# Kernel optimization log

Hardware: AMD Instinct MI355X
Metric: run time of the kernel (lower is better)

Reference implementation:

```python
import jax, jax.numpy as jnp
import numpy as np
from jax import lax

P = 128   # patch_size
S = 64    # stride
K = 31    # PSF kernel size
NZ = 15   # number of Zernike coefficients
HID = 64  # aberration MLP hidden width


def setup_inputs() -> dict:
    key = jax.random.key(0)
    ks = jax.random.split(key, 8)
    B, C, H, W = 8, 3, 512, 512
    x_hat = jax.random.uniform(ks[0], (B, C, H, W), dtype=jnp.float32)
    w1 = jax.random.normal(ks[1], (2, HID), dtype=jnp.float32) * 0.5
    b1 = jnp.zeros((HID,), jnp.float32)
    w2 = jax.random.normal(ks[2], (HID, HID), dtype=jnp.float32) * 0.125
    b2 = jnp.zeros((HID,), jnp.float32)
    w3 = jax.random.normal(ks[3], (HID, NZ), dtype=jnp.float32) * 0.1
    b3 = jnp.zeros((NZ,), jnp.float32)
    zernike_basis = jax.random.normal(ks[4], (NZ, K, K), dtype=jnp.float32) * 0.5
    return {"x_hat": x_hat, "w1": w1, "b1": b1, "w2": w2, "b2": b2,
            "w3": w3, "b3": b3, "zernike_basis": zernike_basis}


def _hann(n):
    # torch.hann_window (periodic=True): 0.5*(1 - cos(2*pi*k/n))
    return 0.5 - 0.5 * jnp.cos(2.0 * jnp.pi * jnp.arange(n, dtype=jnp.float32) / n)


def _psf_from_coeffs(coeffs, basis):
    # coeffs: [N, NZ], basis: [NZ, K, K] -> normalized PSFs [N, K, K]
    phase = jnp.einsum('nz,zhw->nhw', coeffs, basis)          # [N, K, K]
    g = jnp.linspace(-1.0, 1.0, K, dtype=jnp.float32)
    r2 = g[:, None] ** 2 + g[None, :] ** 2
    mask = (r2 <= 1.0).astype(jnp.float32)                    # circular pupil
    pupil = mask * jnp.exp(1j * phase.astype(jnp.complex64))
    field = jnp.fft.fftshift(jnp.fft.fft2(jnp.fft.ifftshift(pupil, axes=(-2, -1))), axes=(-2, -1))
    psf = jnp.abs(field) ** 2
    psf = psf / (jnp.sum(psf, axis=(-2, -1), keepdims=True) + 1e-12)
    return psf


def _forward(x_hat, w1, b1, w2, b2, w3, b3, basis):
    B, C, H, W = x_hat.shape
    pad_h = (S - (H - P) % S) % S
    pad_w = (S - (W - P) % S) % S
    x = jnp.pad(x_hat, ((0, 0), (0, 0), (0, pad_h), (0, pad_w)), mode='reflect') \
        if (pad_h or pad_w) else x_hat
    H_pad, W_pad = x.shape[2], x.shape[3]
    n_h = (H_pad - P) // S + 1
    n_w = (W_pad - P) // S + 1
    N = n_h * n_w

    # ---- unfold into overlapping patches: [B*N, C, P, P] ----
    r0 = jnp.arange(n_h) * S
    c0 = jnp.arange(n_w) * S
    ridx = r0[:, None] + jnp.arange(P)[None, :]               # [n_h, P]
    cidx = c0[:, None] + jnp.arange(P)[None, :]               # [n_w, P]
    patches = x[:, :, ridx[:, None, :, None], cidx[None, :, None, :]]  # [B,C,n_h,n_w,P,P]
    patches = patches.transpose(0, 2, 3, 1, 4, 5).reshape(B * N, C, P, P)

    # ---- per-patch normalized center coords in [-1, 1] ----
    y_norm = (r0.astype(jnp.float32) + P / 2.0) / H_pad * 2.0 - 1.0
    x_norm = (c0.astype(jnp.float32) + P / 2.0) / W_pad * 2.0 - 1.0
    gy, gx = jnp.meshgrid(y_norm, x_norm, indexing='ij')
    coords = jnp.stack([gy, gx], axis=-1).reshape(N, 2)       # [N, 2]
    coords = jnp.tile(coords, (B, 1))                         # [B*N, 2]

    # ---- aberration MLP -> Zernike coeffs -> PSF kernels ----
    h = jax.nn.relu(coords @ w1 + b1)
    h = jax.nn.relu(h @ w2 + b2)
    coeffs = h @ w3 + b3                                      # [B*N, NZ]
    psf = _psf_from_coeffs(coeffs, basis)                     # [B*N, K, K], C_k = 1
    kf = psf[:, ::-1, ::-1]                                   # flip -> true convolution

    # ---- spatially varying per-patch conv (C>1, C_k==1 broadcast branch) ----
    BN = B * N
    pad = K // 2
    xp = jnp.pad(patches, ((0, 0), (0, 0), (pad, pad), (pad, pad)))
    lhs = xp.reshape(1, BN * C, P + 2 * pad, P + 2 * pad)
    rhs = jnp.broadcast_to(kf[:, None, :, :], (BN, C, K, K)).reshape(BN * C, 1, K, K)
    y = lax.conv_general_dilated(lhs, rhs, (1, 1), 'VALID',
                                 dimension_numbers=('NCHW', 'OIHW', 'NCHW'),
                                 feature_group_count=BN * C)
    y_patches = y.reshape(BN, C, P, P)

    # ---- Hann window + overlap-add fold ----
    hann = _hann(P)
    window = hann[:, None] * hann[None, :]                    # [P, P]
    y_patches = y_patches * window[None, None]

    idx = (ridx[:, None, :, None] * W_pad + cidx[None, :, None, :]).reshape(-1)  # [N*P*P]
    vals = y_patches.reshape(B, N, C, P, P).transpose(0, 2, 1, 3, 4).reshape(B, C, -1)
    y_accum = jnp.zeros((B, C, H_pad * W_pad), jnp.float32).at[:, :, idx].add(vals)
    y_accum = y_accum.reshape(B, C, H_pad, W_pad)

    wvals = jnp.broadcast_to(window, (N, P, P)).reshape(-1)
    w_accum = jnp.zeros((H_pad * W_pad,), jnp.float32).at[idx].add(wvals)
    w_accum = w_accum.reshape(1, 1, H_pad, W_pad)

    y_hat = y_accum / (w_accum + 1e-8)
    return y_hat[:, :, :H, :W]


def reference(x_hat, w1, b1, w2, b2, w3, b3, zernike_basis):
    return _forward(x_hat, w1, b1, w2, b2, w3, b3, zernike_basis)
```

## Files before the change

kernel.cpp:

```cpp
#include <hip/hip_runtime.h>
#include <math.h>

#define B_ 8
#define C_ 3
#define HW_ 512
#define P_ 128
#define S_ 64
#define K_ 31
#define NZ_ 15
#define HID_ 64
#define NPOS_ 49
#define BN_ (B_*NPOS_)

#define LROWB_ 384
#define TROWS_ 160
#define FRAG_U32_ 256
#define NSTEP_ 16
#define BPOS_U32_ (NSTEP_ * 3 * FRAG_U32_)

typedef __attribute__((ext_vector_type(8))) short bf16x8;
typedef __attribute__((ext_vector_type(4))) float f32x4;

__device__ __forceinline__ float hann128(int p) {
    return 0.5f - 0.5f * cosf(6.283185307179586f * (float)p / 128.0f);
}

__device__ __forceinline__ unsigned int bf16_rne(float f) {
    union { float f; unsigned int u; } v; v.f = f;
    unsigned int r = v.u + 0x7fffu + ((v.u >> 16) & 1u);
    return r >> 16;
}

__device__ __forceinline__ float bf16_to_f(unsigned int bits16) {
    union { unsigned int u; float f; } v; v.u = bits16 << 16;
    return v.f;
}

__global__ __launch_bounds__(1024) void psf_kernel(
    const float* __restrict__ w1, const float* __restrict__ b1,
    const float* __restrict__ w2, const float* __restrict__ b2,
    const float* __restrict__ w3, const float* __restrict__ b3,
    const float* __restrict__ basis, unsigned int* __restrict__ bfrags)
{
    __shared__ float h1[HID_], h2[HID_], coef[NZ_];
    __shared__ float pupR[961], pupI[961], tR[961], tI[961];
    __shared__ float rootR[31], rootI[31];
    __shared__ float red[16];
    int n = blockIdx.x;
    int nh = n / 7, nw = n % 7;
    int tid = threadIdx.x;
    float cy = (float)(nh * S_ + P_ / 2) * (2.0f / (float)HW_) - 1.0f;
    float cx = (float)(nw * S_ + P_ / 2) * (2.0f / (float)HW_) - 1.0f;

    if (tid < HID_) h1[tid] = fmaxf(0.0f, cy * w1[tid] + cx * w1[HID_ + tid] + b1[tid]);
    if (tid < 31) {
        float ang = -6.283185307179586f * (float)tid / 31.0f;
        rootR[tid] = cosf(ang);
        rootI[tid] = sinf(ang);
    }
    __syncthreads();
    if (tid < HID_) {
        float s = b2[tid];
        for (int k = 0; k < HID_; ++k) s = fmaf(h1[k], w2[k * HID_ + tid], s);
        h2[tid] = fmaxf(0.0f, s);
    }
    __syncthreads();
    if (tid < NZ_) {
        float s = b3[tid];
        for (int k = 0; k < HID_; ++k) s = fmaf(h2[k], w3[k * NZ_ + tid], s);
        coef[tid] = s;
    }
    __syncthreads();

    for (int idx = tid; idx < 961; idx += 1024) {
        int h = idx / 31, w = idx % 31;
        float ph = 0.0f;
        for (int z = 0; z < NZ_; ++z) ph = fmaf(coef[z], basis[z * 961 + idx], ph);
        int dh = h - 15, dw = w - 15;
        bool m = (dh * dh + dw * dw) <= 225;
        float sv, cv;
        sincosf(ph, &sv, &cv);
        pupR[idx] = m ? cv : 0.0f;
        pupI[idx] = m ? sv : 0.0f;
    }
    __syncthreads();

    for (int idx = tid; idx < 961; idx += 1024) {
        int h = idx / 31, k = idx % 31;
        float ar = 0.0f, ai = 0.0f;
        for (int w = 0; w < 31; ++w) {
            int tt = (k * w) % 31;
            float cr = rootR[tt], ci = rootI[tt];
            float pr = pupR[h * 31 + w], pi = pupI[h * 31 + w];
            ar += pr * cr - pi * ci;
            ai += pr * ci + pi * cr;
        }
        tR[idx] = ar; tI[idx] = ai;
    }
    __syncthreads();

    float lsum = 0.0f;
    for (int idx = tid; idx < 961; idx += 1024) {
        int u = idx / 31, k = idx % 31;
        float gr = 0.0f, gi = 0.0f;
        for (int h = 0; h < 31; ++h) {
            int tt = (u * h) % 31;
            float cr = rootR[tt], ci = rootI[tt];
            float ar = tR[h * 31 + k], ai = tI[h * 31 + k];
            gr += ar * cr - ai * ci;
            gi += ar * ci + ai * cr;
        }
        float p = gr * gr + gi * gi;
        pupR[idx] = p;
        lsum += p;
    }
    float v = lsum;
    #pragma unroll
    for (int off = 32; off >= 1; off >>= 1) v += __shfl_xor(v, off, 64);
    if ((tid & 63) == 0) red[tid >> 6] = v;
    __syncthreads();
    if (tid == 0) {
        float s = 0.0f;
        #pragma unroll
        for (int i = 0; i < 16; ++i) s += red[i];
        red[0] = 1.0f / (s + 1e-12f);
    }
    __syncthreads();
    float inv = red[0];
    for (int idx = tid; idx < 961; idx += 1024) {
        int j = idx / 31, i = idx % 31;
        int u = (15 - j + 31) % 31, vv = (15 - i + 31) % 31;
        tI[idx] = pupR[u * 31 + vv] * inv;
    }
    __syncthreads();

    unsigned int* bf = bfrags + (size_t)n * BPOS_U32_;
    for (int w2 = tid; w2 < BPOS_U32_; w2 += 1024) {
        int jc = w2 >> 8;
        int s = jc / 3, c = jc % 3;
        int rem = w2 & 255;
        int l = rem >> 2, ew = rem & 3;
        int nn = l & 15, kg = l >> 4;
        unsigned int pack = 0;
        #pragma unroll
        for (int q = 0; q < 2; ++q) {
            int e = ew * 2 + q;
            int kk = kg * 8 + e;
            int jrow = 2 * s + (kk >> 4);
            int tap = 16 * c + (kk & 15) - nn;
            float vx = (jrow >= 1 && jrow <= 31 && tap >= 1 && tap <= 31)
                       ? tI[(jrow - 1) * 31 + (tap - 1)] : 0.0f;
            pack |= bf16_rne(vx) << (16 * q);
        }
        bf[w2] = pack;
    }
}

template<int MODE>
__global__ __launch_bounds__(512, 4) void conv_mfma_kernel(
    const float* __restrict__ x, const unsigned int* __restrict__ bfrags,
    void* __restrict__ dst)
{
    __shared__ unsigned short sIn[TROWS_ * (LROWB_ / 2)];
    __shared__ float sH[128];

    int t = blockIdx.x;
    int cc = t % 3;
    int bn = t / 3;
    int b = bn / NPOS_, n = bn % NPOS_;
    int nh = n / 7, nw = n % 7;
    int r0 = nh * S_, c0 = nw * S_;
    int tid = threadIdx.x;

    if (tid < 128) sH[tid] = hann128(tid);

    const float* xb = x + ((size_t)(b * C_ + cc) * HW_ + r0) * HW_ + c0;
    for (int i = tid; i < TROWS_ * 24; i += 512) {
        int r = i / 24, jj = i % 24;
        uint4 o = make_uint4(0u, 0u, 0u, 0u);
        if (r >= 16 && r < 144 && jj >= 2 && jj <= 17) {
            const float* rp = &xb[(r - 16) * HW_ + (jj * 8 - 16)];
            float4 v0 = *(const float4*)rp;
            float4 v1 = *(const float4*)(rp + 4);
            o.x = bf16_rne(v0.x) | (bf16_rne(v0.y) << 16);
            o.y = bf16_rne(v0.z) | (bf16_rne(v0.w) << 16);
            o.z = bf16_rne(v1.x) | (bf16_rne(v1.y) << 16);
            o.w = bf16_rne(v1.z) | (bf16_rne(v1.w) << 16);
        }
        int byteoff = (r * LROWB_ + jj * 16) ^ ((r & 7) << 4);
        *(uint4*)((char*)sIn + byteoff) = o;
    }
    __syncthreads();

    int lane = tid & 63, wv = tid >> 6;
    int m0 = wv * 16;
    int lrow = lane & 15, lkg = lane >> 4;

    f32x4 acc[8];
    #pragma unroll
    for (int q = 0; q < 8; ++q) acc[q] = (f32x4){0.f, 0.f, 0.f, 0.f};

    int rowb = m0 + lrow + (lkg >> 1);
    int colb = (lkg & 1) * 16;
    const bf16x8* bpos = (const bf16x8*)(bfrags + (size_t)n * BPOS_U32_) + lane;
    int sbase = wv * 2;

    int ss0 = sbase & 15;
    bf16x8 Bc0 = bpos[ss0 * 192], Bc1 = bpos[ss0 * 192 + 64], Bc2 = bpos[ss0 * 192 + 128];

    #pragma unroll 2
    for (int s = 0; s < NSTEP_; ++s) {
        int ss = (s + sbase) & 15;
        bf16x8 Bn0, Bn1, Bn2;
        if (s + 1 < NSTEP_) {
            int ssn = (s + 1 + sbase) & 15;
            const bf16x8* bp = bpos + ssn * 192;
            Bn0 = bp[0]; Bn1 = bp[64]; Bn2 = bp[128];
        } else { Bn0 = Bc0; Bn1 = Bc1; Bn2 = Bc2; }

        int r2 = rowb + 2 * ss;
        int base = r2 * LROWB_ + colb;
        int xorv = (r2 & 7) << 4;
        bf16x8 A[10];
        #pragma unroll
        for (int p = 0; p < 10; ++p)
            A[p] = *(const bf16x8*)((const char*)sIn + ((base + p * 32) ^ xorv));

        __builtin_amdgcn_s_setprio(1);
        #pragma unroll
        for (int q = 0; q < 8; ++q) {
            acc[q] = __builtin_amdgcn_mfma_f32_16x16x32_bf16(A[q],     Bc0, acc[q], 0, 0, 0);
            acc[q] = __builtin_amdgcn_mfma_f32_16x16x32_bf16(A[q + 1], Bc1, acc[q], 0, 0, 0);
            acc[q] = __builtin_amdgcn_mfma_f32_16x16x32_bf16(A[q + 2], Bc2, acc[q], 0, 0, 0);
        }
        __builtin_amdgcn_s_setprio(0);
        Bc0 = Bn0; Bc1 = Bn1; Bc2 = Bn2;
    }

    int prow0 = m0 + lkg * 4;
    float hy[4];
    #pragma unroll
    for (int r = 0; r < 4; ++r) hy[r] = sH[prow0 + r];

    #pragma unroll
    for (int q = 0; q < 8; ++q) {
        int pcol = 16 * q + lrow;
        float hxv = sH[pcol];
        #pragma unroll
        for (int r = 0; r < 4; ++r) {
            int prow = prow0 + r;
            float val = acc[q][r] * hy[r] * hxv;
            if (MODE == 0) {
                unsigned short* yp = (unsigned short*)dst + (((size_t)bn * C_ + cc) << 14);
                yp[prow * P_ + pcol] = (unsigned short)bf16_rne(val);
            } else {
                float* ob = (float*)dst;
                atomicAdd(ob + ((size_t)(b * C_ + cc) * HW_ + r0 + prow) * HW_ + c0 + pcol, val);
            }
        }
    }
}

__global__ __launch_bounds__(256) void gather_kernel(
    const unsigned short* __restrict__ ypatch, float* __restrict__ out)
{
    __shared__ float sH[128];
    int tid = threadIdx.x;
    if (tid < 128) sH[tid] = hann128(tid);
    __syncthreads();

    int gid = blockIdx.x * 256 + tid;
    int base = gid * 4;
    if (base >= B_ * C_ * HW_ * HW_) return;
    int X = base & 511;
    int Y = (base >> 9) & 511;
    int bc = base >> 18;
    int c = bc % 3, b = bc / 3;
    int nhA = Y >> 6, pyA = Y & 63;
    int nwA = X >> 6, pxA = X & 63;
    bool vA = nhA <= 6, vB = nhA >= 1;
    bool uA = nwA <= 6, uB = nwA >= 1;
    float wy = (vA ? sH[pyA] : 0.0f) + (vB ? sH[pyA + 64] : 0.0f);

    float4 acc = {0.f, 0.f, 0.f, 0.f};
    #pragma unroll
    for (int sy = 0; sy < 2; ++sy) {
        bool okY = sy == 0 ? vA : vB;
        int nh = sy == 0 ? nhA : nhA - 1;
        int py = sy == 0 ? pyA : pyA + 64;
        #pragma unroll
        for (int sx = 0; sx < 2; ++sx) {
            bool okX = sx == 0 ? uA : uB;
            int nw = sx == 0 ? nwA : nwA - 1;
            int px = sx == 0 ? pxA : pxA + 64;
            if (okY && okX) {
                size_t off = ((((size_t)b * NPOS_ + nh * 7 + nw) * C_ + c) << 14) + (py << 7) + px;
                uint2 v = *(const uint2*)&ypatch[off];
                acc.x += bf16_to_f(v.x & 0xffffu);
                acc.y += bf16_to_f(v.x >> 16);
                acc.z += bf16_to_f(v.y & 0xffffu);
                acc.w += bf16_to_f(v.y >> 16);
            }
        }
    }
    float4 o;
    float wx0 = (uA ? sH[pxA + 0] : 0.0f) + (uB ? sH[pxA + 64] : 0.0f);
    float wx1 = (uA ? sH[pxA + 1] : 0.0f) + (uB ? sH[pxA + 65] : 0.0f);
    float wx2 = (uA ? sH[pxA + 2] : 0.0f) + (uB ? sH[pxA + 66] : 0.0f);
    float wx3 = (uA ? sH[pxA + 3] : 0.0f) + (uB ? sH[pxA + 67] : 0.0f);
    o.x = acc.x / (wy * wx0 + 1e-8f);
    o.y = acc.y / (wy * wx1 + 1e-8f);
    o.z = acc.z / (wy * wx2 + 1e-8f);
    o.w = acc.w / (wy * wx3 + 1e-8f);
    *(float4*)&out[base] = o;
}

__global__ __launch_bounds__(256) void divide_kernel(float* __restrict__ out)
{
    int idx = blockIdx.x * 256 + threadIdx.x;
    if (idx >= B_ * C_ * HW_ * HW_) return;
    int X = idx & 511;
    int Y = (idx >> 9) & 511;
    int nhA = Y >> 6, pyA = Y & 63;
    int nwA = X >> 6, pxA = X & 63;
    float wy = (nhA <= 6 ? hann128(pyA) : 0.0f) + (nhA >= 1 ? hann128(pyA + 64) : 0.0f);
    float wx = (nwA <= 6 ? hann128(pxA) : 0.0f) + (nwA >= 1 ? hann128(pxA + 64) : 0.0f);
    out[idx] = out[idx] / (wy * wx + 1e-8f);
}

extern "C" void kernel_launch(void* const* d_in, const int* in_sizes, int n_in,
                              void* d_out, int out_size, void* d_ws, size_t ws_size,
                              hipStream_t stream)
{
    const float* x    = (const float*)d_in[0];
    const float* w1   = (const float*)d_in[1];
    const float* b1   = (const float*)d_in[2];
    const float* w2   = (const float*)d_in[3];
    const float* b2   = (const float*)d_in[4];
    const float* w3   = (const float*)d_in[5];
    const float* b3   = (const float*)d_in[6];
    const float* basis = (const float*)d_in[7];
    float* out = (float*)d_out;

    unsigned int* bfrags = (unsigned int*)d_ws;
    size_t bfBytes = (size_t)NPOS_ * BPOS_U32_ * sizeof(unsigned int);
    size_t need = bfBytes + (size_t)BN_ * C_ * P_ * P_ * sizeof(unsigned short);

    psf_kernel<<<NPOS_, 1024, 0, stream>>>(w1, b1, w2, b2, w3, b3, basis, bfrags);

    int nPix = B_ * C_ * HW_ * HW_;
    if (ws_size >= need) {
        unsigned short* ypatch = (unsigned short*)((char*)d_ws + bfBytes);
        conv_mfma_kernel<0><<<BN_ * C_, 512, 0, stream>>>(x, bfrags, ypatch);
        gather_kernel<<<(nPix / 4 + 255) / 256, 256, 0, stream>>>(ypatch, out);
    } else {
        hipMemsetAsync(d_out, 0, (size_t)out_size * sizeof(float), stream);
        conv_mfma_kernel<1><<<BN_ * C_, 512, 0, stream>>>(x, bfrags, out);
        divide_kernel<<<(nPix + 255) / 256, 256, 0, stream>>>(out);
    }
}
```

Baseline: 79.11 us.

## Fuse patch convolution and overlap-add into per-output-tile kernel

Replaces the per-patch conv kernel, the bf16 patch buffer and the separate gather pass with one kernel per 64x64 output tile. Each tile loads one shared input halo and runs the MFMA convolution against the PSFs of up to four overlapping patches. It then applies the Hann weights and the normalisation divide before a single direct store. This removes the intermediate patch write/read traffic and one kernel launch. In exchange it adds per-tile branching on patch validity and loads B fragments for four positions per step.

```diff
diff --git a/kernel.cpp b/kernel.cpp
--- a/kernel.cpp
+++ b/kernel.cpp
@@ -12,8 +12,8 @@
 #define NPOS_ 49
 #define BN_ (B_*NPOS_)
 
-#define LROWB_ 384
-#define TROWS_ 160
+#define LROWB_ 256
+#define TROWS_ 96
 #define FRAG_U32_ 256
 #define NSTEP_ 16
 #define BPOS_U32_ (NSTEP_ * 3 * FRAG_U32_)
@@ -29,11 +29,6 @@
     union { float f; unsigned int u; } v; v.f = f;
     unsigned int r = v.u + 0x7fffu + ((v.u >> 16) & 1u);
     return r >> 16;
-}
-
-__device__ __forceinline__ float bf16_to_f(unsigned int bits16) {
-    union { unsigned int u; float f; } v; v.u = bits16 << 16;
-    return v.f;
 }
 
 __global__ __launch_bounds__(1024) void psf_kernel(
@@ -156,176 +151,158 @@
     }
 }
 
-template<int MODE>
-__global__ __launch_bounds__(512, 4) void conv_mfma_kernel(
+#define MF(Aop, Bop, Cop) __builtin_amdgcn_mfma_f32_16x16x32_bf16(Aop, Bop, Cop, 0, 0, 0)
+
+__global__ __launch_bounds__(256, 3) void conv_out_kernel(
     const float* __restrict__ x, const unsigned int* __restrict__ bfrags,
-    void* __restrict__ dst)
+    float* __restrict__ out)
 {
     __shared__ unsigned short sIn[TROWS_ * (LROWB_ / 2)];
     __shared__ float sH[128];
 
     int t = blockIdx.x;
-    int cc = t % 3;
-    int bn = t / 3;
-    int b = bn / NPOS_, n = bn % NPOS_;
-    int nh = n / 7, nw = n % 7;
-    int r0 = nh * S_, c0 = nw * S_;
+    int tile = t & 63;
+    int ty = tile >> 3, tx = tile & 7;
+    int bc = t >> 6;
     int tid = threadIdx.x;
 
     if (tid < 128) sH[tid] = hann128(tid);
 
-    const float* xb = x + ((size_t)(b * C_ + cc) * HW_ + r0) * HW_ + c0;
-    for (int i = tid; i < TROWS_ * 24; i += 512) {
-        int r = i / 24, jj = i % 24;
+    const float* xb = x + (size_t)bc * (HW_ * (size_t)HW_);
+    int xr0 = ty * 64 - 16, xc0 = tx * 64 - 16;
+    for (int i = tid; i < TROWS_ * 16; i += 256) {
+        int r = i >> 4, g = i & 15;
+        if (g >= 12) continue;
+        int xr = xr0 + r;
+        int xc = xc0 + g * 8;
         uint4 o = make_uint4(0u, 0u, 0u, 0u);
-        if (r >= 16 && r < 144 && jj >= 2 && jj <= 17) {
-            const float* rp = &xb[(r - 16) * HW_ + (jj * 8 - 16)];
-            float4 v0 = *(const float4*)rp;
-            float4 v1 = *(const float4*)(rp + 4);
-            o.x = bf16_rne(v0.x) | (bf16_rne(v0.y) << 16);
-            o.y = bf16_rne(v0.z) | (bf16_rne(v0.w) << 16);
-            o.z = bf16_rne(v1.x) | (bf16_rne(v1.y) << 16);
-            o.w = bf16_rne(v1.z) | (bf16_rne(v1.w) << 16);
-        }
-        int byteoff = (r * LROWB_ + jj * 16) ^ ((r & 7) << 4);
+        if (xr >= 0 && xr < HW_) {
+            const float* rp = &xb[(size_t)xr * HW_];
+            if (xc >= 0 && xc + 7 < HW_) {
+                float4 v0 = *(const float4*)(rp + xc);
+                float4 v1 = *(const float4*)(rp + xc + 4);
+                o.x = bf16_rne(v0.x) | (bf16_rne(v0.y) << 16);
+                o.y = bf16_rne(v0.z) | (bf16_rne(v0.w) << 16);
+                o.z = bf16_rne(v1.x) | (bf16_rne(v1.y) << 16);
+                o.w = bf16_rne(v1.z) | (bf16_rne(v1.w) << 16);
+            } else {
+                float vv[8];
+                #pragma unroll
+                for (int e = 0; e < 8; ++e) {
+                    int c = xc + e;
+                    vv[e] = (c >= 0 && c < HW_) ? rp[c] : 0.0f;
+                }
+                o.x = bf16_rne(vv[0]) | (bf16_rne(vv[1]) << 16);
+                o.y = bf16_rne(vv[2]) | (bf16_rne(vv[3]) << 16);
+                o.z = bf16_rne(vv[4]) | (bf16_rne(vv[5]) << 16);
+                o.w = bf16_rne(vv[6]) | (bf16_rne(vv[7]) << 16);
+            }
+        }
+        int byteoff = (r * LROWB_ + g * 16) ^ ((r & 7) << 4);
         *(uint4*)((char*)sIn + byteoff) = o;
     }
     __syncthreads();
 
+    bool vy0 = (ty >= 1), vy1 = (ty <= 6);
+    bool vx0 = (tx >= 1), vx1 = (tx <= 6);
+    bool pv0 = vy0 && vx0, pv1 = vy0 && vx1, pv2 = vy1 && vx0, pv3 = vy1 && vx1;
     int lane = tid & 63, wv = tid >> 6;
+    int n0 = pv0 ? ((ty - 1) * 7 + (tx - 1)) : 0;
+    int n1 = pv1 ? ((ty - 1) * 7 + tx) : 0;
+    int n2 = pv2 ? (ty * 7 + (tx - 1)) : 0;
+    int n3 = pv3 ? (ty * 7 + tx) : 0;
+    const bf16x8* bp0 = (const bf16x8*)(bfrags + (size_t)n0 * BPOS_U32_) + lane;
+    const bf16x8* bp1 = (const bf16x8*)(bfrags + (size_t)n1 * BPOS_U32_) + lane;
+    const bf16x8* bp2 = (const bf16x8*)(bfrags + (size_t)n2 * BPOS_U32_) + lane;
+    const bf16x8* bp3 = (const bf16x8*)(bfrags + (size_t)n3 * BPOS_U32_) + lane;
+
     int m0 = wv * 16;
     int lrow = lane & 15, lkg = lane >> 4;
-
-    f32x4 acc[8];
+    int rowb = m0 + lrow + (lkg >> 1);
+    int cb16 = (lkg & 1) * 16;
+
+    f32x4 acc[4][4];
     #pragma unroll
-    for (int q = 0; q < 8; ++q) acc[q] = (f32x4){0.f, 0.f, 0.f, 0.f};
-
-    int rowb = m0 + lrow + (lkg >> 1);
-    int colb = (lkg & 1) * 16;
-    const bf16x8* bpos = (const bf16x8*)(bfrags + (size_t)n * BPOS_U32_) + lane;
-    int sbase = wv * 2;
-
-    int ss0 = sbase & 15;
-    bf16x8 Bc0 = bpos[ss0 * 192], Bc1 = bpos[ss0 * 192 + 64], Bc2 = bpos[ss0 * 192 + 128];
+    for (int p = 0; p < 4; ++p)
+        #pragma unroll
+        for (int q = 0; q < 4; ++q) acc[p][q] = (f32x4){0.f, 0.f, 0.f, 0.f};
+
+    const bf16x8 ZV = {0, 0, 0, 0, 0, 0, 0, 0};
 
     #pragma unroll 2
     for (int s = 0; s < NSTEP_; ++s) {
-        int ss = (s + sbase) & 15;
-        bf16x8 Bn0, Bn1, Bn2;
-        if (s + 1 < NSTEP_) {
-            int ssn = (s + 1 + sbase) & 15;
-            const bf16x8* bp = bpos + ssn * 192;
-            Bn0 = bp[0]; Bn1 = bp[64]; Bn2 = bp[128];
-        } else { Bn0 = Bc0; Bn1 = Bc1; Bn2 = Bc2; }
-
-        int r2 = rowb + 2 * ss;
-        int base = r2 * LROWB_ + colb;
+        int r2 = rowb + 2 * s;
+        int base = r2 * LROWB_ + cb16;
         int xorv = (r2 & 7) << 4;
-        bf16x8 A[10];
-        #pragma unroll
-        for (int p = 0; p < 10; ++p)
-            A[p] = *(const bf16x8*)((const char*)sIn + ((base + p * 32) ^ xorv));
-
-        __builtin_amdgcn_s_setprio(1);
-        #pragma unroll
-        for (int q = 0; q < 8; ++q) {
-            acc[q] = __builtin_amdgcn_mfma_f32_16x16x32_bf16(A[q],     Bc0, acc[q], 0, 0, 0);
-            acc[q] = __builtin_amdgcn_mfma_f32_16x16x32_bf16(A[q + 1], Bc1, acc[q], 0, 0, 0);
-            acc[q] = __builtin_amdgcn_mfma_f32_16x16x32_bf16(A[q + 2], Bc2, acc[q], 0, 0, 0);
-        }
-        __builtin_amdgcn_s_setprio(0);
-        Bc0 = Bn0; Bc1 = Bn1; Bc2 = Bn2;
+        bf16x8 A[6];
+        #pragma unroll
+        for (int w = 0; w < 6; ++w)
+            A[w] = *(const bf16x8*)((const char*)sIn + ((base + 32 * w) ^ xorv));
+        bool okLo = (r2 < 80);
+        bool okHi = (r2 >= 16);
+        bf16x8 Alo[6], Ahi[6];
+        #pragma unroll
+        for (int w = 0; w < 6; ++w) {
+            Alo[w] = okLo ? A[w] : ZV;
+            Ahi[w] = okHi ? A[w] : ZV;
+        }
+
+        if (pv0) {
+            const bf16x8* bb = bp0 + s * 192;
+            bf16x8 B0 = bb[0], B1 = bb[64], B2 = bb[128];
+            acc[0][0] = MF(Alo[0], B0, acc[0][0]); acc[0][0] = MF(Alo[1], B1, acc[0][0]); acc[0][0] = MF(Alo[2], B2, acc[0][0]);
+            acc[0][1] = MF(Alo[1], B0, acc[0][1]); acc[0][1] = MF(Alo[2], B1, acc[0][1]); acc[0][1] = MF(Alo[3], B2, acc[0][1]);
+            acc[0][2] = MF(Alo[2], B0, acc[0][2]); acc[0][2] = MF(Alo[3], B1, acc[0][2]); acc[0][2] = MF(Alo[4], B2, acc[0][2]);
+            acc[0][3] = MF(Alo[3], B0, acc[0][3]); acc[0][3] = MF(Alo[4], B1, acc[0][3]);
+        }
+        if (pv1) {
+            const bf16x8* bb = bp1 + s * 192;
+            bf16x8 B0 = bb[0], B1 = bb[64], B2 = bb[128];
+            acc[1][0] = MF(Alo[1], B1, acc[1][0]); acc[1][0] = MF(Alo[2], B2, acc[1][0]);
+            acc[1][1] = MF(Alo[1], B0, acc[1][1]); acc[1][1] = MF(Alo[2], B1, acc[1][1]); acc[1][1] = MF(Alo[3], B2, acc[1][1]);
+            acc[1][2] = MF(Alo[2], B0, acc[1][2]); acc[1][2] = MF(Alo[3], B1, acc[1][2]); acc[1][2] = MF(Alo[4], B2, acc[1][2]);
+            acc[1][3] = MF(Alo[3], B0, acc[1][3]); acc[1][3] = MF(Alo[4], B1, acc[1][3]); acc[1][3] = MF(Alo[5], B2, acc[1][3]);
+        }
+        if (pv2) {
+            const bf16x8* bb = bp2 + s * 192;
+            bf16x8 B0 = bb[0], B1 = bb[64], B2 = bb[128];
+            acc[2][0] = MF(Ahi[0], B0, acc[2][0]); acc[2][0] = MF(Ahi[1], B1, acc[2][0]); acc[2][0] = MF(Ahi[2], B2, acc[2][0]);
+            acc[2][1] = MF(Ahi[1], B0, acc[2][1]); acc[2][1] = MF(Ahi[2], B1, acc[2][1]); acc[2][1] = MF(Ahi[3], B2, acc[2][1]);
+            acc[2][2] = MF(Ahi[2], B0, acc[2][2]); acc[2][2] = MF(Ahi[3], B1, acc[2][2]); acc[2][2] = MF(Ahi[4], B2, acc[2][2]);
+            acc[2][3] = MF(Ahi[3], B0, acc[2][3]); acc[2][3] = MF(Ahi[4], B1, acc[2][3]);
+        }
+        if (pv3) {
+            const bf16x8* bb = bp3 + s * 192;
+            bf16x8 B0 = bb[0], B1 = bb[64], B2 = bb[128];
+            acc[3][0] = MF(Ahi[1], B1, acc[3][0]); acc[3][0] = MF(Ahi[2], B2, acc[3][0]);
+            acc[3][1] = MF(Ahi[1], B0, acc[3][1]); acc[3][1] = MF(Ahi[2], B1, acc[3][1]); acc[3][1] = MF(Ahi[3], B2, acc[3][1]);
+            acc[3][2] = MF(Ahi[2], B0, acc[3][2]); acc[3][2] = MF(Ahi[3], B1, acc[3][2]); acc[3][2] = MF(Ahi[4], B2, acc[3][2]);
+            acc[3][3] = MF(Ahi[3], B0, acc[3][3]); acc[3][3] = MF(Ahi[4], B1, acc[3][3]); acc[3][3] = MF(Ahi[5], B2, acc[3][3]);
+        }
     }
 
     int prow0 = m0 + lkg * 4;
-    float hy[4];
+    float* ob = out + (size_t)bc * (HW_ * (size_t)HW_) + (size_t)(ty * 64) * HW_ + tx * 64;
     #pragma unroll
-    for (int r = 0; r < 4; ++r) hy[r] = sH[prow0 + r];
-
-    #pragma unroll
-    for (int q = 0; q < 8; ++q) {
+    for (int q = 0; q < 4; ++q) {
         int pcol = 16 * q + lrow;
-        float hxv = sH[pcol];
+        float hx1 = sH[pcol];
+        float hx0 = sH[pcol + 64];
+        float wx = (vx0 ? hx0 : 0.0f) + (vx1 ? hx1 : 0.0f);
         #pragma unroll
         for (int r = 0; r < 4; ++r) {
             int prow = prow0 + r;
-            float val = acc[q][r] * hy[r] * hxv;
-            if (MODE == 0) {
-                unsigned short* yp = (unsigned short*)dst + (((size_t)bn * C_ + cc) << 14);
-                yp[prow * P_ + pcol] = (unsigned short)bf16_rne(val);
-            } else {
-                float* ob = (float*)dst;
-                atomicAdd(ob + ((size_t)(b * C_ + cc) * HW_ + r0 + prow) * HW_ + c0 + pcol, val);
-            }
-        }
-    }
-}
-
-__global__ __launch_bounds__(256) void gather_kernel(
-    const unsigned short* __restrict__ ypatch, float* __restrict__ out)
-{
-    __shared__ float sH[128];
-    int tid = threadIdx.x;
-    if (tid < 128) sH[tid] = hann128(tid);
-    __syncthreads();
-
-    int gid = blockIdx.x * 256 + tid;
-    int base = gid * 4;
-    if (base >= B_ * C_ * HW_ * HW_) return;
-    int X = base & 511;
-    int Y = (base >> 9) & 511;
-    int bc = base >> 18;
-    int c = bc % 3, b = bc / 3;
-    int nhA = Y >> 6, pyA = Y & 63;
-    int nwA = X >> 6, pxA = X & 63;
-    bool vA = nhA <= 6, vB = nhA >= 1;
-    bool uA = nwA <= 6, uB = nwA >= 1;
-    float wy = (vA ? sH[pyA] : 0.0f) + (vB ? sH[pyA + 64] : 0.0f);
-
-    float4 acc = {0.f, 0.f, 0.f, 0.f};
-    #pragma unroll
-    for (int sy = 0; sy < 2; ++sy) {
-        bool okY = sy == 0 ? vA : vB;
-        int nh = sy == 0 ? nhA : nhA - 1;
-        int py = sy == 0 ? pyA : pyA + 64;
-        #pragma unroll
-        for (int sx = 0; sx < 2; ++sx) {
-            bool okX = sx == 0 ? uA : uB;
-            int nw = sx == 0 ? nwA : nwA - 1;
-            int px = sx == 0 ? pxA : pxA + 64;
-            if (okY && okX) {
-                size_t off = ((((size_t)b * NPOS_ + nh * 7 + nw) * C_ + c) << 14) + (py << 7) + px;
-                uint2 v = *(const uint2*)&ypatch[off];
-                acc.x += bf16_to_f(v.x & 0xffffu);
-                acc.y += bf16_to_f(v.x >> 16);
-                acc.z += bf16_to_f(v.y & 0xffffu);
-                acc.w += bf16_to_f(v.y >> 16);
-            }
-        }
-    }
-    float4 o;
-    float wx0 = (uA ? sH[pxA + 0] : 0.0f) + (uB ? sH[pxA + 64] : 0.0f);
-    float wx1 = (uA ? sH[pxA + 1] : 0.0f) + (uB ? sH[pxA + 65] : 0.0f);
-    float wx2 = (uA ? sH[pxA + 2] : 0.0f) + (uB ? sH[pxA + 66] : 0.0f);
-    float wx3 = (uA ? sH[pxA + 3] : 0.0f) + (uB ? sH[pxA + 67] : 0.0f);
-    o.x = acc.x / (wy * wx0 + 1e-8f);
-    o.y = acc.y / (wy * wx1 + 1e-8f);
-    o.z = acc.z / (wy * wx2 + 1e-8f);
-    o.w = acc.w / (wy * wx3 + 1e-8f);
-    *(float4*)&out[base] = o;
-}
-
-__global__ __launch_bounds__(256) void divide_kernel(float* __restrict__ out)
-{
-    int idx = blockIdx.x * 256 + threadIdx.x;
-    if (idx >= B_ * C_ * HW_ * HW_) return;
-    int X = idx & 511;
-    int Y = (idx >> 9) & 511;
-    int nhA = Y >> 6, pyA = Y & 63;
-    int nwA = X >> 6, pxA = X & 63;
-    float wy = (nhA <= 6 ? hann128(pyA) : 0.0f) + (nhA >= 1 ? hann128(pyA + 64) : 0.0f);
-    float wx = (nwA <= 6 ? hann128(pxA) : 0.0f) + (nwA >= 1 ? hann128(pxA + 64) : 0.0f);
-    out[idx] = out[idx] / (wy * wx + 1e-8f);
+            float hy1 = sH[prow];
+            float hy0 = sH[prow + 64];
+            float wy = (vy0 ? hy0 : 0.0f) + (vy1 ? hy1 : 0.0f);
+            float val = 0.0f;
+            if (pv0) val += acc[0][q][r] * hy0 * hx0;
+            if (pv1) val += acc[1][q][r] * hy0 * hx1;
+            if (pv2) val += acc[2][q][r] * hy1 * hx0;
+            if (pv3) val += acc[3][q][r] * hy1 * hx1;
+            ob[prow * HW_ + pcol] = val / (wy * wx + 1e-8f);
+        }
+    }
 }
 
 extern "C" void kernel_launch(void* const* d_in, const int* in_sizes, int n_in,
@@ -343,19 +320,7 @@
     float* out = (float*)d_out;
 
     unsigned int* bfrags = (unsigned int*)d_ws;
-    size_t bfBytes = (size_t)NPOS_ * BPOS_U32_ * sizeof(unsigned int);
-    size_t need = bfBytes + (size_t)BN_ * C_ * P_ * P_ * sizeof(unsigned short);
 
     psf_kernel<<<NPOS_, 1024, 0, stream>>>(w1, b1, w2, b2, w3, b3, basis, bfrags);
-
-    int nPix = B_ * C_ * HW_ * HW_;
-    if (ws_size >= need) {
-        unsigned short* ypatch = (unsigned short*)((char*)d_ws + bfBytes);
-        conv_mfma_kernel<0><<<BN_ * C_, 512, 0, stream>>>(x, bfrags, ypatch);
-        gather_kernel<<<(nPix / 4 + 255) / 256, 256, 0, stream>>>(ypatch, out);
-    } else {
-        hipMemsetAsync(d_out, 0, (size_t)out_size * sizeof(float), stream);
-        conv_mfma_kernel<1><<<BN_ * C_, 512, 0, stream>>>(x, bfrags, out);
-        divide_kernel<<<(nPix + 255) / 256, 256, 0, stream>>>(out);
-    }
-}
+    conv_out_kernel<<<B_ * C_ * 64, 256, 0, stream>>>(x, bfrags, out);
+}
```

Result: slower. 90.39 us (+14.3%).
